# Kernel tuning notes

Hardware: AMD Instinct MI355X
Metric: run time of the kernel (lower is better)

## Reference

```python
import jax, jax.numpy as jnp
import numpy as np

BETA = 0.25  # commitment loss weight


def setup_inputs() -> dict:
    key = jax.random.key(0)
    k1, k2 = jax.random.split(key)
    x = jax.random.normal(k1, (64, 64, 64, 64), dtype=jnp.float32)
    # embeddings: [embedding_dim=64, num_embeddings=512], random_uniform init in [-0.05, 0.05]
    embeddings = jax.random.uniform(k2, (64, 512), dtype=jnp.float32, minval=-0.05, maxval=0.05)
    return {"x": x, "embeddings": embeddings}


def reference(x, embeddings):
    d = embeddings.shape[0]
    flat = x.reshape(-1, d)                                   # [N, D]
    # squared L2 distances to each code: ||z||^2 + ||e||^2 - 2 z.e
    sim = flat @ embeddings                                   # [N, K]
    dist = (jnp.sum(flat * flat, axis=1, keepdims=True)
            + jnp.sum(embeddings * embeddings, axis=0)
            - 2.0 * sim)                                      # [N, K]
    idx = jnp.argmin(dist, axis=1)                            # [N]
    # gather nearest code (equivalent to one_hot @ embeddings.T)
    quantized = jnp.take(embeddings.T, idx, axis=0).reshape(x.shape)
    commitment_loss = jnp.mean((jax.lax.stop_gradient(quantized) - x) ** 2)
    codebook_loss = jnp.mean((quantized - jax.lax.stop_gradient(x)) ** 2)
    loss = BETA * commitment_loss + codebook_loss
    # straight-through estimator
    quantized_st = x + jax.lax.stop_gradient(quantized - x)
    return quantized_st, loss
```

## Files before the change

### kernel.cpp

```cpp
#include <hip/hip_runtime.h>


#define NROWS 262144
#define D 64
#define K 512
#define MARGIN 0.09f
#define INF32 3.4e38f

#define WS_ET 0
#define WS_E2 131072
#define WS_EBT 133120
#define WS_PARTIALS 198656

typedef __attribute__((ext_vector_type(8))) short bf16x8;
typedef __attribute__((ext_vector_type(4))) float f32x4;

union ClRed { unsigned cl[2048]; double red[512]; };

__device__ inline unsigned short f2bf(float f) {
    unsigned u = __float_as_uint(f);
    u += 0x7fffu + ((u >> 16) & 1u);
    return (unsigned short)(u >> 16);
}
__device__ inline unsigned pack_bf2(float lo, float hi) {
    unsigned ulo = __float_as_uint(lo); ulo += 0x7fffu + ((ulo >> 16) & 1u);
    unsigned uhi = __float_as_uint(hi); uhi += 0x7fffu + ((uhi >> 16) & 1u);
    return (ulo >> 16) | (uhi & 0xffff0000u);
}
__device__ inline bf16x8 pack8(float4 p, float4 q) {
    union { unsigned u[4]; bf16x8 v; } r;
    r.u[0] = pack_bf2(p.x, p.y); r.u[1] = pack_bf2(p.z, p.w);
    r.u[2] = pack_bf2(q.x, q.y); r.u[3] = pack_bf2(q.z, q.w);
    return r.v;
}

__global__ void __launch_bounds__(64) vq_prep(const float* __restrict__ emb, char* ws) {
    float* e2 = (float*)(ws + WS_E2);
    float* et = (float*)(ws + WS_ET);
    unsigned short* ebT = (unsigned short*)(ws + WS_EBT);
    int k = blockIdx.x * 64 + threadIdx.x;
    float v0 = emb[k];
    et[k * D] = v0;
    ebT[k * D] = f2bf(v0);
    float s = __fmul_rn(v0, v0);
    for (int d = 1; d < D; ++d) {
        float v = emb[d * K + k];
        et[k * D + d] = v;
        ebT[k * D + d] = f2bf(v);
        s = __fadd_rn(s, __fmul_rn(v, v));
    }
    e2[k] = s;
}

__device__ __noinline__ unsigned long long exact_pack(
        const float* __restrict__ x, const float* __restrict__ et,
        const float* __restrict__ e2f, int row, int k) {
    const float* xr = x + (size_t)row * D;
    float r0 = __fmul_rn(xr[0], xr[0]), r1 = __fmul_rn(xr[1], xr[1]);
    float r2 = __fmul_rn(xr[2], xr[2]), r3 = __fmul_rn(xr[3], xr[3]);
    float r4 = __fmul_rn(xr[4], xr[4]), r5 = __fmul_rn(xr[5], xr[5]);
    float r6 = __fmul_rn(xr[6], xr[6]), r7 = __fmul_rn(xr[7], xr[7]);
    for (int i = 8; i < 64; i += 8) {
        r0 = __fadd_rn(r0, __fmul_rn(xr[i],     xr[i]));
        r1 = __fadd_rn(r1, __fmul_rn(xr[i + 1], xr[i + 1]));
        r2 = __fadd_rn(r2, __fmul_rn(xr[i + 2], xr[i + 2]));
        r3 = __fadd_rn(r3, __fmul_rn(xr[i + 3], xr[i + 3]));
        r4 = __fadd_rn(r4, __fmul_rn(xr[i + 4], xr[i + 4]));
        r5 = __fadd_rn(r5, __fmul_rn(xr[i + 5], xr[i + 5]));
        r6 = __fadd_rn(r6, __fmul_rn(xr[i + 6], xr[i + 6]));
        r7 = __fadd_rn(r7, __fmul_rn(xr[i + 7], xr[i + 7]));
    }
    float z2 = __fadd_rn(__fadd_rn(__fadd_rn(r0, r1), __fadd_rn(r2, r3)),
                         __fadd_rn(__fadd_rn(r4, r5), __fadd_rn(r6, r7)));
    const float* ep = et + (size_t)k * D;
    float a = 0.f;
    for (int d = 0; d < D; ++d) a = fmaf(xr[d], ep[d], a);
    float dist = __fsub_rn(__fadd_rn(z2, e2f[k]), __fmul_rn(2.0f, a));
    return ((unsigned long long)__float_as_uint(dist) << 32) | (unsigned)k;
}

__global__ void __launch_bounds__(512)
vq_fused(const float* __restrict__ x, float* __restrict__ out,
         char* __restrict__ ws) {
    const float* et  = (const float*)(ws + WS_ET);
    const float* e2f = (const float*)(ws + WS_E2);
    const unsigned short* ebT = (const unsigned short*)(ws + WS_EBT);
    double* partials = (double*)(ws + WS_PARTIALS);

    __shared__ unsigned short ebs[32768];
    __shared__ float le2[512];
    __shared__ unsigned long long lgmin[256];
    __shared__ ClRed u;
    __shared__ int ccnt;
    __shared__ int ovf;

    const int tid = threadIdx.x;
    const int wv = tid >> 6, lane = tid & 63;
    const int c15 = lane & 15;
    const int g = lane >> 4;
    const int kofs = g * 8;
    const int gr4 = g * 4;
    const int bswz = ((int)blockIdx.x & 7) * 128 + ((int)blockIdx.x >> 3);
    const int blockRow0 = bswz * 256;
    const int rowBase = blockRow0 + wv * 32;

    if (tid < 256) lgmin[tid] = 0xFFFFFFFFFFFFFFFFULL;
    if (tid == 0) { ccnt = 0; ovf = 0; }
    if (tid < 512) le2[tid] = e2f[tid];

    {
        const uint4* src = (const uint4*)ebT;
        uint4* dstv = (uint4*)ebs;
        for (int i = tid; i < 4096; i += 512) {
            int row = i >> 3, s = i & 7;
            dstv[(row << 3) + (s ^ (row & 7))] = src[i];
        }
    }

    bf16x8 aA0, aA1, aB0, aB1;
#define LOADA(RT, A0, A1) { \
    const float* xp = x + ((size_t)(rowBase + (RT) * 16 + c15)) * D + kofs; \
    float4 p0 = *(const float4*)xp; \
    float4 p1 = *(const float4*)(xp + 4); \
    float4 p2 = *(const float4*)(xp + 32); \
    float4 p3 = *(const float4*)(xp + 36); \
    A0 = pack8(p0, p1); A1 = pack8(p2, p3); }
    LOADA(0, aA0, aA1) LOADA(1, aB0, aB1)
#undef LOADA

    __syncthreads();

    float m00 = INF32, m01 = INF32, m02 = INF32, m03 = INF32;
    float m10 = INF32, m11 = INF32, m12 = INF32, m13 = INF32;

#define SW1(A0, A1, M0, M1, M2, M3) { \
    f32x4 acc = {0.f, 0.f, 0.f, 0.f}; \
    acc = __builtin_amdgcn_mfma_f32_16x16x32_bf16(A0, bb0, acc, 0, 0, 0); \
    acc = __builtin_amdgcn_mfma_f32_16x16x32_bf16(A1, bb1, acc, 0, 0, 0); \
    M0 = fminf(M0, fmaf(-2.0f, acc[0], e2c)); \
    M1 = fminf(M1, fmaf(-2.0f, acc[1], e2c)); \
    M2 = fminf(M2, fmaf(-2.0f, acc[2], e2c)); \
    M3 = fminf(M3, fmaf(-2.0f, acc[3], e2c)); }

    for (int j = 0; j < 32; ++j) {
        const int kkl = j * 16 + c15;
        const int rsw = kkl & 7;
        const unsigned short* bp = ebs + (kkl << 6);
        bf16x8 bb0 = *(const bf16x8*)(bp + ((g ^ rsw) << 3));
        bf16x8 bb1 = *(const bf16x8*)(bp + (((g + 4) ^ rsw) << 3));
        float e2c = le2[kkl];
        SW1(aA0, aA1, m00, m01, m02, m03)
        SW1(aB0, aB1, m10, m11, m12, m13)
    }
#undef SW1

#define RED(v) v = fminf(v, __shfl_xor(v, 1)); v = fminf(v, __shfl_xor(v, 2)); \
               v = fminf(v, __shfl_xor(v, 4)); v = fminf(v, __shfl_xor(v, 8)); \
               v += MARGIN;
    RED(m00) RED(m01) RED(m02) RED(m03)
    RED(m10) RED(m11) RED(m12) RED(m13)
#undef RED

#define PUSH(RT, R) { int idx = atomicAdd(&ccnt, 1); \
    if (idx < 2048) u.cl[idx] = \
        ((unsigned)(wv * 32 + (RT) * 16 + gr4 + (R)) << 9) | (unsigned)kkl; \
    else ovf = 1; }

#define SW2(RT, A0, A1, M0, M1, M2, M3) { \
    f32x4 acc = {0.f, 0.f, 0.f, 0.f}; \
    acc = __builtin_amdgcn_mfma_f32_16x16x32_bf16(A0, bb0, acc, 0, 0, 0); \
    acc = __builtin_amdgcn_mfma_f32_16x16x32_bf16(A1, bb1, acc, 0, 0, 0); \
    if (fmaf(-2.0f, acc[0], e2c) <= M0) PUSH(RT, 0) \
    if (fmaf(-2.0f, acc[1], e2c) <= M1) PUSH(RT, 1) \
    if (fmaf(-2.0f, acc[2], e2c) <= M2) PUSH(RT, 2) \
    if (fmaf(-2.0f, acc[3], e2c) <= M3) PUSH(RT, 3) }

    for (int j = 0; j < 32; ++j) {
        const int kkl = j * 16 + c15;
        const int rsw = kkl & 7;
        const unsigned short* bp = ebs + (kkl << 6);
        bf16x8 bb0 = *(const bf16x8*)(bp + ((g ^ rsw) << 3));
        bf16x8 bb1 = *(const bf16x8*)(bp + (((g + 4) ^ rsw) << 3));
        float e2c = le2[kkl];
        SW2(0, aA0, aA1, m00, m01, m02, m03)
        SW2(1, aB0, aB1, m10, m11, m12, m13)
    }
#undef SW2
#undef PUSH

    __syncthreads();
    const int cnt = (ccnt < 2048) ? ccnt : 2048;
    for (int i = tid; i < cnt; i += 512) {
        unsigned e = u.cl[i];
        int rowLocal = (int)(e >> 9);
        int k = (int)(e & 0x1ffu);
        atomicMin(&lgmin[rowLocal], exact_pack(x, et, e2f, blockRow0 + rowLocal, k));
    }
    if (ovf) {
        for (int p = tid; p < 256 * 512; p += 512)
            atomicMin(&lgmin[p >> 9],
                      exact_pack(x, et, e2f, blockRow0 + (p >> 9), p & 0x1ff));
    }
    __syncthreads();

    const int rowL = tid >> 1;
    const int half = tid & 1;
    const int row = blockRow0 + rowL;
    const int kb = (int)(lgmin[rowL] & 0xFFFFFFFFULL);
    const float4* cq = (const float4*)(et + (size_t)kb * D) + half * 8;
    const float4* xr = (const float4*)(x + (size_t)row * D) + half * 8;
    float4* outr = (float4*)(out + (size_t)row * D) + half * 8;
    double rs = 0.0;
#define OUTQ(G) { \
        float4 e4 = cq[G]; float4 xv = xr[G]; float4 o; \
        float d0 = __fsub_rn(e4.x, xv.x); \
        float d1 = __fsub_rn(e4.y, xv.y); \
        float d2 = __fsub_rn(e4.z, xv.z); \
        float d3 = __fsub_rn(e4.w, xv.w); \
        o.x = __fadd_rn(xv.x, d0); \
        o.y = __fadd_rn(xv.y, d1); \
        o.z = __fadd_rn(xv.z, d2); \
        o.w = __fadd_rn(xv.w, d3); \
        outr[G] = o; \
        rs += (double)__fmul_rn(d0, d0) + (double)__fmul_rn(d1, d1) + \
              (double)__fmul_rn(d2, d2) + (double)__fmul_rn(d3, d3); }
    OUTQ(0) OUTQ(1) OUTQ(2) OUTQ(3) OUTQ(4) OUTQ(5) OUTQ(6) OUTQ(7)
#undef OUTQ

    u.red[tid] = rs;
    __syncthreads();
    for (int s = 256; s > 0; s >>= 1) {
        if (tid < s) u.red[tid] += u.red[tid + s];
        __syncthreads();
    }
    if (tid == 0) partials[bswz] = u.red[0];
}

__global__ void __launch_bounds__(256) vq_finalize(float* __restrict__ out, char* ws) {
    const double* partials = (const double*)(ws + WS_PARTIALS);
    __shared__ double red[256];
    double s = partials[threadIdx.x] + partials[threadIdx.x + 256] +
               partials[threadIdx.x + 512] + partials[threadIdx.x + 768];
    red[threadIdx.x] = s;
    __syncthreads();
    for (int st = 128; st > 0; st >>= 1) {
        if (threadIdx.x < st) red[threadIdx.x] += red[threadIdx.x + st];
        __syncthreads();
    }
    if (threadIdx.x == 0) {
        out[16777216] = (float)(1.25 * red[0] / 16777216.0);
    }
}

extern "C" void kernel_launch(void* const* d_in, const int* in_sizes, int n_in,
                              void* d_out, int out_size, void* d_ws, size_t ws_size,
                              hipStream_t stream) {
    const float* x   = (const float*)d_in[0];
    const float* emb = (const float*)d_in[1];
    float* out = (float*)d_out;
    char* ws = (char*)d_ws;

    vq_prep<<<8, 64, 0, stream>>>(emb, ws);
    vq_fused<<<NROWS / 256, 512, 0, stream>>>(x, out, ws);
    vq_finalize<<<1, 256, 0, stream>>>(out, ws);
}
```

Before: 184.1 us.

## Stage codebook into LDS in two halves and prefetch next B fragment

```diff
diff --git a/kernel.cpp b/kernel.cpp
--- a/kernel.cpp
+++ b/kernel.cpp
@@ -87,7 +87,7 @@
     const unsigned short* ebT = (const unsigned short*)(ws + WS_EBT);
     double* partials = (double*)(ws + WS_PARTIALS);
 
-    __shared__ unsigned short ebs[32768];
+    __shared__ unsigned short ebs[16384];
     __shared__ float le2[512];
     __shared__ unsigned long long lgmin[256];
     __shared__ ClRed u;
@@ -106,16 +106,7 @@
 
     if (tid < 256) lgmin[tid] = 0xFFFFFFFFFFFFFFFFULL;
     if (tid == 0) { ccnt = 0; ovf = 0; }
-    if (tid < 512) le2[tid] = e2f[tid];
-
-    {
-        const uint4* src = (const uint4*)ebT;
-        uint4* dstv = (uint4*)ebs;
-        for (int i = tid; i < 4096; i += 512) {
-            int row = i >> 3, s = i & 7;
-            dstv[(row << 3) + (s ^ (row & 7))] = src[i];
-        }
-    }
+    le2[tid & 511] = e2f[tid & 511];
 
     bf16x8 aA0, aA1, aB0, aB1;
 #define LOADA(RT, A0, A1) { \
@@ -128,7 +119,15 @@
     LOADA(0, aA0, aA1) LOADA(1, aB0, aB1)
 #undef LOADA
 
-    __syncthreads();
+#define STAGE(h) { \
+    const uint4* src = (const uint4*)ebT + ((h) << 11); \
+    uint4* dstv = (uint4*)ebs; \
+    _Pragma("unroll") \
+    for (int i = 0; i < 4; ++i) { \
+        int c = i * 512 + tid; \
+        int row = c >> 3, s = c & 7; \
+        dstv[(row << 3) + (s ^ (row & 7))] = src[c]; \
+    } }
 
     float m00 = INF32, m01 = INF32, m02 = INF32, m03 = INF32;
     float m10 = INF32, m11 = INF32, m12 = INF32, m13 = INF32;
@@ -142,15 +141,26 @@
     M2 = fminf(M2, fmaf(-2.0f, acc[2], e2c)); \
     M3 = fminf(M3, fmaf(-2.0f, acc[3], e2c)); }
 
-    for (int j = 0; j < 32; ++j) {
-        const int kkl = j * 16 + c15;
-        const int rsw = kkl & 7;
-        const unsigned short* bp = ebs + (kkl << 6);
-        bf16x8 bb0 = *(const bf16x8*)(bp + ((g ^ rsw) << 3));
-        bf16x8 bb1 = *(const bf16x8*)(bp + (((g + 4) ^ rsw) << 3));
-        float e2c = le2[kkl];
-        SW1(aA0, aA1, m00, m01, m02, m03)
-        SW1(aB0, aB1, m10, m11, m12, m13)
+    for (int h = 0; h < 2; ++h) {
+        __syncthreads();
+        STAGE(h)
+        __syncthreads();
+        bf16x8 bb0, bb1;
+        {
+            const unsigned short* bp = ebs + (c15 << 6);
+            bb0 = *(const bf16x8*)(bp + ((g ^ (c15 & 7)) << 3));
+            bb1 = *(const bf16x8*)(bp + (((g + 4) ^ (c15 & 7)) << 3));
+        }
+        for (int j = 0; j < 16; ++j) {
+            const int nkl = ((j + 1) & 15) * 16 + c15;
+            const unsigned short* np = ebs + (nkl << 6);
+            bf16x8 nb0 = *(const bf16x8*)(np + ((g ^ (nkl & 7)) << 3));
+            bf16x8 nb1 = *(const bf16x8*)(np + (((g + 4) ^ (nkl & 7)) << 3));
+            float e2c = le2[(h << 8) + j * 16 + c15];
+            SW1(aA0, aA1, m00, m01, m02, m03)
+            SW1(aB0, aB1, m10, m11, m12, m13)
+            bb0 = nb0; bb1 = nb1;
+        }
     }
 #undef SW1
 
@@ -163,7 +173,7 @@
 
 #define PUSH(RT, R) { int idx = atomicAdd(&ccnt, 1); \
     if (idx < 2048) u.cl[idx] = \
-        ((unsigned)(wv * 32 + (RT) * 16 + gr4 + (R)) << 9) | (unsigned)kkl; \
+        ((unsigned)(wv * 32 + (RT) * 16 + gr4 + (R)) << 9) | (unsigned)kg; \
     else ovf = 1; }
 
 #define SW2(RT, A0, A1, M0, M1, M2, M3) { \
@@ -175,18 +185,31 @@
     if (fmaf(-2.0f, acc[2], e2c) <= M2) PUSH(RT, 2) \
     if (fmaf(-2.0f, acc[3], e2c) <= M3) PUSH(RT, 3) }
 
-    for (int j = 0; j < 32; ++j) {
-        const int kkl = j * 16 + c15;
-        const int rsw = kkl & 7;
-        const unsigned short* bp = ebs + (kkl << 6);
-        bf16x8 bb0 = *(const bf16x8*)(bp + ((g ^ rsw) << 3));
-        bf16x8 bb1 = *(const bf16x8*)(bp + (((g + 4) ^ rsw) << 3));
-        float e2c = le2[kkl];
-        SW2(0, aA0, aA1, m00, m01, m02, m03)
-        SW2(1, aB0, aB1, m10, m11, m12, m13)
+    for (int h = 0; h < 2; ++h) {
+        __syncthreads();
+        STAGE(h)
+        __syncthreads();
+        bf16x8 bb0, bb1;
+        {
+            const unsigned short* bp = ebs + (c15 << 6);
+            bb0 = *(const bf16x8*)(bp + ((g ^ (c15 & 7)) << 3));
+            bb1 = *(const bf16x8*)(bp + (((g + 4) ^ (c15 & 7)) << 3));
+        }
+        for (int j = 0; j < 16; ++j) {
+            const int nkl = ((j + 1) & 15) * 16 + c15;
+            const unsigned short* np = ebs + (nkl << 6);
+            bf16x8 nb0 = *(const bf16x8*)(np + ((g ^ (nkl & 7)) << 3));
+            bf16x8 nb1 = *(const bf16x8*)(np + (((g + 4) ^ (nkl & 7)) << 3));
+            const int kg = (h << 8) + j * 16 + c15;
+            float e2c = le2[kg];
+            SW2(0, aA0, aA1, m00, m01, m02, m03)
+            SW2(1, aB0, aB1, m10, m11, m12, m13)
+            bb0 = nb0; bb1 = nb1;
+        }
     }
 #undef SW2
 #undef PUSH
+#undef STAGE
 
     __syncthreads();
     const int cnt = (ccnt < 2048) ? ccnt : 2048;
```

Result: slower. 192.7 us (+4.7%).
